# Kernel tuning notes

Hardware: AMD Instinct MI355X
Metric: run time of the kernel (lower is better)

## Reference

```python
import jax, jax.numpy as jnp
import numpy as np

N = 50000
E = 800000
IN_DIM, HID, HEADS, OUT = 128, 32, 8, 64
NEG_SLOPE = 0.2
EPS = 1e-16


def setup_inputs() -> dict:
    key = jax.random.key(0)
    ks = jax.random.split(key, 10)
    return {
        "x": jax.random.normal(ks[0], (N, IN_DIM), dtype=jnp.float32),
        "edge_index": jax.random.randint(ks[1], (2, E), 0, N, dtype=jnp.int64)
        if jax.config.jax_enable_x64 else jax.random.randint(ks[1], (2, E), 0, N, dtype=jnp.int32),
        "W1": jax.random.normal(ks[2], (HEADS * HID, IN_DIM), dtype=jnp.float32) * 0.1,
        "att_src1": jax.random.normal(ks[3], (HEADS, HID), dtype=jnp.float32) * 0.1,
        "att_dst1": jax.random.normal(ks[4], (HEADS, HID), dtype=jnp.float32) * 0.1,
        "b1": jnp.zeros((HEADS * HID,), dtype=jnp.float32),
        "W2": jax.random.normal(ks[5], (OUT, HEADS * HID), dtype=jnp.float32) * 0.1,
        "att_src2": jax.random.normal(ks[6], (1, OUT), dtype=jnp.float32) * 0.1,
        "att_dst2": jax.random.normal(ks[7], (1, OUT), dtype=jnp.float32) * 0.1,
        "b2": jnp.zeros((OUT,), dtype=jnp.float32),
    }


def _gat_conv(x, src, dst, W, att_src, att_dst, bias, heads, out_dim, concat, n_nodes):
    # x: [N, F_in]; W: [heads*out_dim, F_in]; att_*: [heads, out_dim]
    h = (x @ W.T).reshape(n_nodes, heads, out_dim)      # [N, H, D]
    a_src = jnp.einsum('nhd,hd->nh', h, att_src)         # [N, H]
    a_dst = jnp.einsum('nhd,hd->nh', h, att_dst)
    alpha = jax.nn.leaky_relu(a_src[src] + a_dst[dst], NEG_SLOPE)  # [E, H]
    # segment softmax over edges grouped by destination node
    m = jax.ops.segment_max(alpha, dst, num_segments=n_nodes)
    alpha = jnp.exp(alpha - m[dst])
    s = jax.ops.segment_sum(alpha, dst, num_segments=n_nodes)
    alpha = alpha / (s[dst] + EPS)
    msg = h[src] * alpha[:, :, None]                     # [E, H, D]
    out = jax.ops.segment_sum(msg, dst, num_segments=n_nodes)  # [N, H, D]
    if concat:
        out = out.reshape(n_nodes, heads * out_dim)
    else:
        out = out.mean(axis=1)
    return out + bias


def reference(x, edge_index, W1, att_src1, att_dst1, b1, W2, att_src2, att_dst2, b2):
    n = x.shape[0]
    loop = jnp.arange(n, dtype=edge_index.dtype)
    src = jnp.concatenate([edge_index[0], loop])  # PyG add_self_loops=True
    dst = jnp.concatenate([edge_index[1], loop])
    h = _gat_conv(x, src, dst, W1, att_src1, att_dst1, b1, HEADS, HID, True, n)
    h = jax.nn.relu(h)
    out = _gat_conv(h, src, dst, W2, att_src2, att_dst2, b2, 1, OUT, False, n)
    return out
```

## Files before the change

kernel.cpp:

```cpp
#include <hip/hip_runtime.h>
#include <hip/hip_fp16.h>

#define NN 50000
#define EE 800000
#define ET (EE + NN)
#define IND 128
#define F1 256
#define H1 8
#define D1 32
#define F2 64
#define NEG 0.2f
#define EPSV 1e-16f

#define MG2 391
#define NBE 3321
#define BCAP 64

typedef _Float16 half8_t __attribute__((ext_vector_type(8)));
typedef float floatx4 __attribute__((ext_vector_type(4)));

#define W1N4 (256 * 128 / 4)
#define W2N4 (64 * 256 / 4)
__global__ void k_cvtW(const float* __restrict__ w1, const float* __restrict__ w2,
                       __half* __restrict__ w1p, __half* __restrict__ w2h) {
  int i = blockIdx.x * blockDim.x + threadIdx.x;
  if (i < W1N4) {
    float4 v = *(const float4*)(w1 + (size_t)i * 4);
    int col = i >> 5;
    int kb = (i * 4) & 127;
    int by = col >> 7, t = (col >> 4) & 7, ar = col & 15;
    int kk = kb >> 5, ag = (kb >> 3) & 3, j = kb & 7;
    int fid = (by * 8 + t) * 4 + kk;
    int lane = ag * 16 + ar;
    __half2 p0 = __floats2half2_rn(v.x, v.y);
    __half2 p1 = __floats2half2_rn(v.z, v.w);
    float2 st;
    *(__half2*)&st.x = p0;
    *(__half2*)&st.y = p1;
    *(float2*)(w1p + fid * 512 + lane * 8 + j) = st;
    return;
  }
  i -= W1N4;
  if (i >= W2N4) return;
  float4 v = *(const float4*)(w2 + (size_t)i * 4);
  __half2 p0 = __floats2half2_rn(v.x, v.y);
  __half2 p1 = __floats2half2_rn(v.z, v.w);
  float2 st;
  *(__half2*)&st.x = p0;
  *(__half2*)&st.y = p1;
  *(float2*)(w2h + (size_t)i * 4) = st;
}

__global__ __launch_bounds__(256) void k_scg1(const int* __restrict__ ei,
    int* __restrict__ deg, int* __restrict__ bkt,
    const float* __restrict__ A, const __half* __restrict__ Bp,
    __half* __restrict__ Ch) {
  if (blockIdx.x < NBE) {
    int e = blockIdx.x * 256 + threadIdx.x;
    if (e >= ET) return;
    int s, d;
    if (e < EE) { s = ei[e]; d = ei[EE + e]; }
    else        { s = e - EE; d = s; }
    int pos = atomicAdd(&deg[d], 1);
    if (pos < BCAP) bkt[(d << 6) + pos] = s;
    return;
  }
  int b = blockIdx.x - NBE;
  int bx = b % MG2, by = b / MG2;
  int tid = threadIdx.x;
  int wv = tid >> 6, lane = tid & 63;
  int m0 = bx * 128 + wv * 16;
  int ar = lane & 15, ag = lane >> 4;
  int r0 = m0 + ar;       if (r0 >= NN) r0 = NN - 1;
  int r1 = m0 + 64 + ar;  if (r1 >= NN) r1 = NN - 1;
  const float* A0 = A + (size_t)r0 * IND + ag * 8;
  const float* A1 = A + (size_t)r1 * IND + ag * 8;
  floatx4 acc[2][8];
#pragma unroll
  for (int rt = 0; rt < 2; ++rt)
#pragma unroll
    for (int t = 0; t < 8; ++t) acc[rt][t] = (floatx4){0.f, 0.f, 0.f, 0.f};
#pragma unroll
  for (int kk = 0; kk < 4; ++kk) {
    int k0 = kk * 32;
    float4 a00 = *(const float4*)(A0 + k0);
    float4 a01 = *(const float4*)(A0 + k0 + 4);
    float4 a10 = *(const float4*)(A1 + k0);
    float4 a11 = *(const float4*)(A1 + k0 + 4);
    half8_t af0, af1;
    af0[0] = (_Float16)a00.x; af0[1] = (_Float16)a00.y;
    af0[2] = (_Float16)a00.z; af0[3] = (_Float16)a00.w;
    af0[4] = (_Float16)a01.x; af0[5] = (_Float16)a01.y;
    af0[6] = (_Float16)a01.z; af0[7] = (_Float16)a01.w;
    af1[0] = (_Float16)a10.x; af1[1] = (_Float16)a10.y;
    af1[2] = (_Float16)a10.z; af1[3] = (_Float16)a10.w;
    af1[4] = (_Float16)a11.x; af1[5] = (_Float16)a11.y;
    af1[6] = (_Float16)a11.z; af1[7] = (_Float16)a11.w;
#pragma unroll
    for (int t = 0; t < 8; ++t) {
      int fid = (by * 8 + t) * 4 + kk;
      half8_t bf = *(const half8_t*)(Bp + fid * 512 + lane * 8);
      acc[0][t] = __builtin_amdgcn_mfma_f32_16x16x32_f16(af0, bf, acc[0][t], 0, 0, 0);
      acc[1][t] = __builtin_amdgcn_mfma_f32_16x16x32_f16(af1, bf, acc[1][t], 0, 0, 0);
    }
  }
#pragma unroll
  for (int rt = 0; rt < 2; ++rt)
#pragma unroll
    for (int t = 0; t < 8; ++t) {
      int col = by * 128 + t * 16 + ar;
#pragma unroll
      for (int r = 0; r < 4; ++r) {
        int m = m0 + rt * 64 + ag * 4 + r;
        if (m < NN) Ch[(size_t)m * F1 + col] = __float2half(acc[rt][t][r]);
      }
    }
}

template<int H, int D>
__global__ void k_att2(const __half* __restrict__ h, const float* __restrict__ atts,
                       const float* __restrict__ attd, float* __restrict__ as_,
                       float* __restrict__ ad_) {
  const int F = H * D;
  const int CPR = F / 8;
  const int NPW = 64 / CPR;
  const int CPH = D / 8;
  int lane = threadIdx.x & 63;
  int wv = threadIdx.x >> 6;
  int n = blockIdx.x * (4 * NPW) + wv * NPW + lane / CPR;
  if (n >= NN) return;
  int c = lane % CPR;
  int head = c / CPH;
  int within = c % CPH;
  half8_t f = *(const half8_t*)(h + (size_t)n * F + c * 8);
  float s_ = 0.f, d_ = 0.f;
#pragma unroll
  for (int j = 0; j < 8; ++j) {
    float fv = (float)f[j];
    s_ += fv * atts[head * D + within * 8 + j];
    d_ += fv * attd[head * D + within * 8 + j];
  }
#pragma unroll
  for (int m = 1; m < CPH; m <<= 1) {
    s_ += __shfl_xor(s_, m);
    d_ += __shfl_xor(d_, m);
  }
  if (within == 0) {
    as_[n * H + head] = s_;
    ad_[n * H + head] = d_;
  }
}

__global__ __launch_bounds__(256) void k_agg1(const int* __restrict__ deg,
    const int* __restrict__ bkt, const __half* __restrict__ feat,
    const float* __restrict__ as_, const float* __restrict__ ad_,
    const float* __restrict__ bias, __half* __restrict__ outh) {
  int wid = threadIdx.x >> 6;
  int lane = threadIdx.x & 63;
  int d = blockIdx.x * 4 + wid;
  if (d >= NN) return;
  const int b = lane >> 5;
  const int q = lane & 31;
  const int h = q >> 2;
  const int sw = lane >> 3;
  const int hw = lane & 7;
  const char* fb = (const char*)feat;
  float adw = ad_[d * 8 + hw];
  float acc[8] = {};
  float wsacc = 0.f;
  int p0 = d << 6;
  int dg = deg[d];
  int p1 = p0 + dg;
  int nfull = dg >> 3;
  int p = p0;
  for (int it = 0; it < nfull; ++it, p += 8) {
    int sW = bkt[p + sw];
    float t = as_[sW * 8 + hw] + adw;
    t = (t > 0.f) ? t : NEG * t;
    float w = __expf(t);
    wsacc += w;
    int wbits = __float_as_int(w);
#pragma unroll
    for (int i = 0; i < 4; ++i) {
      int slot = 2 * i + b;
      int se = __builtin_amdgcn_ds_bpermute(slot * 32, sW);
      float wv = __int_as_float(
          __builtin_amdgcn_ds_bpermute((slot * 8 + h) * 4, wbits));
      half8_t f = *(const half8_t*)(fb + ((se << 9) | (q << 4)));
#pragma unroll
      for (int j = 0; j < 8; ++j) acc[j] = fmaf(wv, (float)f[j], acc[j]);
    }
  }
  if (p < p1) {
    int pw = p + sw;
    bool v = pw < p1;
    int sW = bkt[v ? pw : (p1 - 1)];
    float t = as_[sW * 8 + hw] + adw;
    t = (t > 0.f) ? t : NEG * t;
    float w = v ? __expf(t) : 0.f;
    wsacc += w;
    int wbits = __float_as_int(w);
#pragma unroll
    for (int i = 0; i < 4; ++i) {
      int slot = 2 * i + b;
      int se = __builtin_amdgcn_ds_bpermute(slot * 32, sW);
      float wv = __int_as_float(
          __builtin_amdgcn_ds_bpermute((slot * 8 + h) * 4, wbits));
      half8_t f = *(const half8_t*)(fb + ((se << 9) | (q << 4)));
#pragma unroll
      for (int j = 0; j < 8; ++j) acc[j] = fmaf(wv, (float)f[j], acc[j]);
    }
  }
  wsacc += __shfl_xor(wsacc, 8);
  wsacc += __shfl_xor(wsacc, 16);
  wsacc += __shfl_xor(wsacc, 32);
  float wst = __int_as_float(
      __builtin_amdgcn_ds_bpermute(h * 4, __float_as_int(wsacc)));
#pragma unroll
  for (int j = 0; j < 8; ++j) acc[j] += __shfl_xor(acc[j], 32);
  if (b == 0) {
    float inv = 1.f / (wst + EPSV);
    __half2 packs[4];
#pragma unroll
    for (int j = 0; j < 8; j += 2) {
      float o0 = fmaxf(fmaf(acc[j], inv, 0.f) + bias[q * 8 + j], 0.f);
      float o1 = fmaxf(fmaf(acc[j + 1], inv, 0.f) + bias[q * 8 + j + 1], 0.f);
      packs[j >> 1] = __floats2half2_rn(o0, o1);
    }
    *(float4*)(outh + (size_t)d * 256 + q * 8) = *(float4*)packs;
  }
}

__global__ __launch_bounds__(256) void k_g2att(const __half* __restrict__ A,
    const __half* __restrict__ Bh, __half* __restrict__ Ch,
    const float* __restrict__ as2w, const float* __restrict__ ad2w,
    float* __restrict__ as2, float* __restrict__ ad2) {
  __shared__ __half Bs[64][256 + 8];
  int tid = threadIdx.x;
  const float4* src = (const float4*)Bh;
  for (int i = tid; i < 64 * 256 / 8; i += 256) {
    int row = i / 32, kc = i % 32;
    *(float4*)&Bs[row][kc * 8] = src[i];
  }
  __syncthreads();
  int wv = tid >> 6, lane = tid & 63;
  int m0 = blockIdx.x * 128 + wv * 16;
  int ar = lane & 15, ag = lane >> 4;
  int r0 = m0 + ar;       if (r0 >= NN) r0 = NN - 1;
  int r1 = m0 + 64 + ar;  if (r1 >= NN) r1 = NN - 1;
  const __half* A0 = A + (size_t)r0 * F1 + ag * 8;
  const __half* A1 = A + (size_t)r1 * F1 + ag * 8;
  floatx4 acc[2][4];
#pragma unroll
  for (int rt = 0; rt < 2; ++rt)
#pragma unroll
    for (int t = 0; t < 4; ++t) acc[rt][t] = (floatx4){0.f, 0.f, 0.f, 0.f};
#pragma unroll
  for (int k0 = 0; k0 < F1; k0 += 32) {
    half8_t af0 = *(const half8_t*)(A0 + k0);
    half8_t af1 = *(const half8_t*)(A1 + k0);
#pragma unroll
    for (int t = 0; t < 4; ++t) {
      half8_t bf = *(const half8_t*)&Bs[t * 16 + ar][k0 + ag * 8];
      acc[0][t] = __builtin_amdgcn_mfma_f32_16x16x32_f16(af0, bf, acc[0][t], 0, 0, 0);
      acc[1][t] = __builtin_amdgcn_mfma_f32_16x16x32_f16(af1, bf, acc[1][t], 0, 0, 0);
    }
  }
  float sp[2][4] = {}, dp[2][4] = {};
#pragma unroll
  for (int t = 0; t < 4; ++t) {
    int col = t * 16 + ar;
    float ws = as2w[col], wd = ad2w[col];
#pragma unroll
    for (int rt = 0; rt < 2; ++rt)
#pragma unroll
      for (int r = 0; r < 4; ++r) {
        int m = m0 + rt * 64 + ag * 4 + r;
        if (m < NN) Ch[(size_t)m * F2 + col] = __float2half(acc[rt][t][r]);
        sp[rt][r] = fmaf(acc[rt][t][r], ws, sp[rt][r]);
        dp[rt][r] = fmaf(acc[rt][t][r], wd, dp[rt][r]);
      }
  }
#pragma unroll
  for (int msk = 1; msk < 16; msk <<= 1)
#pragma unroll
    for (int rt = 0; rt < 2; ++rt)
#pragma unroll
      for (int r = 0; r < 4; ++r) {
        sp[rt][r] += __shfl_xor(sp[rt][r], msk);
        dp[rt][r] += __shfl_xor(dp[rt][r], msk);
      }
  if (ar == 0) {
#pragma unroll
    for (int rt = 0; rt < 2; ++rt)
#pragma unroll
      for (int r = 0; r < 4; ++r) {
        int m = m0 + rt * 64 + ag * 4 + r;
        if (m < NN) { as2[m] = sp[rt][r]; ad2[m] = dp[rt][r]; }
      }
  }
}

__global__ __launch_bounds__(256) void k_agg2(const int* __restrict__ deg,
    const int* __restrict__ bkt, const __half* __restrict__ feat ,
    const float* __restrict__ as_, const float* __restrict__ ad_,
    const float* __restrict__ bias, float* __restrict__ out) {
  int wid = threadIdx.x >> 6;
  int lane = threadIdx.x & 63;
  int d = blockIdx.x * 4 + wid;
  if (d >= NN) return;
  const int b = lane >> 3;
  const int q = lane & 7;
  const char* fb = (const char*)feat;
  float adv = ad_[d];
  float acc[8] = {};
  float ws = 0.f;
  int p0 = d << 6;
  int dg = deg[d];
  int p1 = p0 + dg;
  int nfull = dg >> 3;
  int p = p0;
  for (int it = 0; it < nfull; ++it, p += 8) {
    int se = bkt[p + b];
    float t = as_[se] + adv;
    t = (t > 0.f) ? t : NEG * t;
    float w = __expf(t);
    ws += w;
    half8_t f = *(const half8_t*)(fb + ((se << 7) | (q << 4)));
#pragma unroll
    for (int j = 0; j < 8; ++j) acc[j] = fmaf(w, (float)f[j], acc[j]);
  }
  if (p < p1) {
    int pe = p + b;
    bool v = pe < p1;
    int se = bkt[v ? pe : (p1 - 1)];
    float t = as_[se] + adv;
    t = (t > 0.f) ? t : NEG * t;
    float w = v ? __expf(t) : 0.f;
    ws += w;
    half8_t f = *(const half8_t*)(fb + ((se << 7) | (q << 4)));
#pragma unroll
    for (int j = 0; j < 8; ++j) acc[j] = fmaf(w, (float)f[j], acc[j]);
  }
  ws += __shfl_xor(ws, 8);
  ws += __shfl_xor(ws, 16);
  ws += __shfl_xor(ws, 32);
#pragma unroll
  for (int j = 0; j < 8; ++j) {
    acc[j] += __shfl_xor(acc[j], 8);
    acc[j] += __shfl_xor(acc[j], 16);
    acc[j] += __shfl_xor(acc[j], 32);
  }
  if (b == 0) {
    float inv = 1.f / (ws + EPSV);
    float o[8];
#pragma unroll
    for (int j = 0; j < 8; ++j) o[j] = acc[j] * inv + bias[q * 8 + j];
    *(float4*)(out + (size_t)d * 64 + q * 8) = *(float4*)&o[0];
    *(float4*)(out + (size_t)d * 64 + q * 8 + 4) = *(float4*)&o[4];
  }
}

extern "C" void kernel_launch(void* const* d_in, const int* in_sizes, int n_in,
                              void* d_out, int out_size, void* d_ws, size_t ws_size,
                              hipStream_t stream) {
  const float* x    = (const float*)d_in[0];
  const int*   ei   = (const int*)d_in[1];
  const float* W1   = (const float*)d_in[2];
  const float* as1w = (const float*)d_in[3];
  const float* ad1w = (const float*)d_in[4];
  const float* b1   = (const float*)d_in[5];
  const float* W2   = (const float*)d_in[6];
  const float* as2w = (const float*)d_in[7];
  const float* ad2w = (const float*)d_in[8];
  const float* b2   = (const float*)d_in[9];
  float* out = (float*)d_out;

  char* W = (char*)d_ws;
  __half* h1h = (__half*)W; W += (size_t)NN * 256 * 2;
  __half* h2h = (__half*)W; W += (size_t)NN * 256 * 2;
  __half* hmh = (__half*)W; W += (size_t)NN * 64 * 2;
  __half* W1p = (__half*)W; W += 256 * 128 * 2;
  __half* W2h = (__half*)W; W += 64 * 256 * 2;
  float* as1 = (float*)W; W += (size_t)NN * 8 * 4;
  float* ad1 = (float*)W; W += (size_t)NN * 8 * 4;
  float* as2 = (float*)W; W += (size_t)NN * 4;
  float* ad2 = (float*)W; W += (size_t)NN * 4;
  int* deg    = (int*)W;  W += (size_t)NN * 4;
  int* bkt    = (int*)W;  W += (size_t)NN * BCAP * 4;

  hipMemsetAsync(deg, 0, NN * sizeof(int), stream);

  k_cvtW<<<(W1N4 + W2N4 + 255) / 256, 256, 0, stream>>>(W1, W2, W1p, W2h);
  k_scg1<<<NBE + 2 * MG2, 256, 0, stream>>>(ei, deg, bkt, x, W1p, h1h);
  k_att2<H1, D1><<<(NN + 7) / 8, 256, 0, stream>>>(h1h, as1w, ad1w, as1, ad1);
  k_agg1<<<(NN + 3) / 4, 256, 0, stream>>>(deg, bkt, h1h, as1, ad1, b1, h2h);
  k_g2att<<<MG2, 256, 0, stream>>>(h2h, W2h, hmh, as2w, ad2w, as2, ad2);
  k_agg2<<<(NN + 3) / 4, 256, 0, stream>>>(deg, bkt, hmh, as2, ad2, b2, out);
}
```

Before: 208.6 us.

## Store edge buckets as 16-bit indices and batch edge scatter eight per thread

Bucket source indices are now stored as unsigned short, which is valid because N is below 65536. This halves the bucket footprint that the scatter writes and both aggregation kernels read. The edge-scatter part of the fused kernel now handles eight edges per thread with int4 vector loads, and the GEMM blocks are placed first in the grid so they get scheduled before the atomic scatter blocks. The 16-bit storage ties correctness to node counts below 65536.

Measured after the change: 176.9 us. -15.2%, faster.

```diff
diff --git a/kernel.cpp b/kernel.cpp
--- a/kernel.cpp
+++ b/kernel.cpp
@@ -13,7 +13,7 @@
 #define EPSV 1e-16f
 
 #define MG2 391
-#define NBE 3321
+#define SCB ((ET + 2047) / 2048)
 #define BCAP 64
 
 typedef _Float16 half8_t __attribute__((ext_vector_type(8)));
@@ -52,21 +52,38 @@
 }
 
 __global__ __launch_bounds__(256) void k_scg1(const int* __restrict__ ei,
-    int* __restrict__ deg, int* __restrict__ bkt,
+    int* __restrict__ deg, unsigned short* __restrict__ bkt,
     const float* __restrict__ A, const __half* __restrict__ Bp,
     __half* __restrict__ Ch) {
-  if (blockIdx.x < NBE) {
-    int e = blockIdx.x * 256 + threadIdx.x;
-    if (e >= ET) return;
-    int s, d;
-    if (e < EE) { s = ei[e]; d = ei[EE + e]; }
-    else        { s = e - EE; d = s; }
-    int pos = atomicAdd(&deg[d], 1);
-    if (pos < BCAP) bkt[(d << 6) + pos] = s;
+  if (blockIdx.x >= 2 * MG2) {
+    int base = (blockIdx.x - 2 * MG2) * 2048 + threadIdx.x * 8;
+    if (base >= ET) return;
+    if (base + 8 <= EE) {
+      int4 s0 = *(const int4*)(ei + base);
+      int4 s1 = *(const int4*)(ei + base + 4);
+      int4 d0 = *(const int4*)(ei + EE + base);
+      int4 d1 = *(const int4*)(ei + EE + base + 4);
+      int s[8] = {s0.x, s0.y, s0.z, s0.w, s1.x, s1.y, s1.z, s1.w};
+      int d[8] = {d0.x, d0.y, d0.z, d0.w, d1.x, d1.y, d1.z, d1.w};
+#pragma unroll
+      for (int j = 0; j < 8; ++j) {
+        int pos = atomicAdd(&deg[d[j]], 1);
+        if (pos < BCAP) bkt[(d[j] << 6) + pos] = (unsigned short)s[j];
+      }
+    } else {
+      for (int j = 0; j < 8; ++j) {
+        int e = base + j;
+        if (e >= ET) break;
+        int ss, dd;
+        if (e < EE) { ss = ei[e]; dd = ei[EE + e]; }
+        else        { ss = e - EE; dd = ss; }
+        int pos = atomicAdd(&deg[dd], 1);
+        if (pos < BCAP) bkt[(dd << 6) + pos] = (unsigned short)ss;
+      }
+    }
     return;
   }
-  int b = blockIdx.x - NBE;
-  int bx = b % MG2, by = b / MG2;
+  int bx = blockIdx.x % MG2, by = blockIdx.x / MG2;
   int tid = threadIdx.x;
   int wv = tid >> 6, lane = tid & 63;
   int m0 = bx * 128 + wv * 16;
@@ -152,7 +169,7 @@
 }
 
 __global__ __launch_bounds__(256) void k_agg1(const int* __restrict__ deg,
-    const int* __restrict__ bkt, const __half* __restrict__ feat,
+    const unsigned short* __restrict__ bkt, const __half* __restrict__ feat,
     const float* __restrict__ as_, const float* __restrict__ ad_,
     const float* __restrict__ bias, __half* __restrict__ outh) {
   int wid = threadIdx.x >> 6;
@@ -302,7 +319,7 @@
 }
 
 __global__ __launch_bounds__(256) void k_agg2(const int* __restrict__ deg,
-    const int* __restrict__ bkt, const __half* __restrict__ feat ,
+    const unsigned short* __restrict__ bkt, const __half* __restrict__ feat,
     const float* __restrict__ as_, const float* __restrict__ ad_,
     const float* __restrict__ bias, float* __restrict__ out) {
   int wid = threadIdx.x >> 6;
@@ -387,12 +404,12 @@
   float* as2 = (float*)W; W += (size_t)NN * 4;
   float* ad2 = (float*)W; W += (size_t)NN * 4;
   int* deg    = (int*)W;  W += (size_t)NN * 4;
-  int* bkt    = (int*)W;  W += (size_t)NN * BCAP * 4;
+  unsigned short* bkt = (unsigned short*)W; W += (size_t)NN * BCAP * 2;
 
   hipMemsetAsync(deg, 0, NN * sizeof(int), stream);
 
   k_cvtW<<<(W1N4 + W2N4 + 255) / 256, 256, 0, stream>>>(W1, W2, W1p, W2h);
-  k_scg1<<<NBE + 2 * MG2, 256, 0, stream>>>(ei, deg, bkt, x, W1p, h1h);
+  k_scg1<<<2 * MG2 + SCB, 256, 0, stream>>>(ei, deg, bkt, x, W1p, h1h);
   k_att2<H1, D1><<<(NN + 7) / 8, 256, 0, stream>>>(h1h, as1w, ad1w, as1, ad1);
   k_agg1<<<(NN + 3) / 4, 256, 0, stream>>>(deg, bkt, h1h, as1, ad1, b1, h2h);
   k_g2att<<<MG2, 256, 0, stream>>>(h2h, W2h, hmh, as2w, ad2w, as2, ad2);
```
